# Kernel optimization log

Hardware: AMD Instinct MI355X
Metric: run time of the kernel (lower is better)

The kernel has to match this reference:

```python
import jax, jax.numpy as jnp
import numpy as np

N_NODES = 50000
N_EDGES = 1600000
NODE_DIM = 64
HIDDEN_DIM = 128
EDGE_DIM = 32


def _linear_params(key, fan_in, fan_out, bias=True):
    k1, k2 = jax.random.split(key)
    bound = 1.0 / np.sqrt(fan_in)
    W = jax.random.uniform(k1, (fan_in, fan_out), minval=-bound, maxval=bound, dtype=jnp.float32)
    if bias:
        b = jax.random.uniform(k2, (fan_out,), minval=-bound, maxval=bound, dtype=jnp.float32)
        return W, b
    return W, None


def setup_inputs() -> dict:
    key = jax.random.key(0)
    ks = jax.random.split(key, 12)
    h = jax.random.normal(ks[0], (N_NODES, NODE_DIM), dtype=jnp.float32)
    x = jax.random.normal(ks[1], (N_NODES, 3), dtype=jnp.float32) * 10.0
    edge_index = jax.random.randint(ks[2], (2, N_EDGES), 0, N_NODES, dtype=jnp.int32).astype(jnp.int64)
    edge_dist = jax.random.uniform(ks[3], (N_EDGES,), dtype=jnp.float32) * 10.0

    msg_in = 2 * NODE_DIM + EDGE_DIM
    node_w1, node_b1 = _linear_params(ks[4], msg_in, HIDDEN_DIM)
    node_w2, node_b2 = _linear_params(ks[5], HIDDEN_DIM, NODE_DIM)
    coord_w1, coord_b1 = _linear_params(ks[6], msg_in, HIDDEN_DIM)
    coord_w2, _ = _linear_params(ks[7], HIDDEN_DIM, 1, bias=False)
    edge_w1, edge_b1 = _linear_params(ks[8], 1, EDGE_DIM)
    edge_w2, edge_b2 = _linear_params(ks[9], EDGE_DIM, EDGE_DIM)

    return dict(h=h, x=x, edge_index=edge_index, edge_dist=edge_dist,
                node_w1=node_w1, node_b1=node_b1, node_w2=node_w2, node_b2=node_b2,
                coord_w1=coord_w1, coord_b1=coord_b1, coord_w2=coord_w2,
                edge_w1=edge_w1, edge_b1=edge_b1, edge_w2=edge_w2, edge_b2=edge_b2)


def reference(h, x, edge_index, edge_dist,
              node_w1, node_b1, node_w2, node_b2,
              coord_w1, coord_b1, coord_w2,
              edge_w1, edge_b1, edge_w2, edge_b2):
    src = edge_index[0]
    dst = edge_index[1]

    # edge_mlp: Linear(1, edge_dim) -> SiLU -> Linear(edge_dim, edge_dim)
    edge_attr = jax.nn.silu(edge_dist[:, None] @ edge_w1 + edge_b1) @ edge_w2 + edge_b2

    # per-edge message input: [E, 2*node_dim + edge_dim]
    m_input = jnp.concatenate([h[src], h[dst], edge_attr], axis=-1)

    # node_mlp: Linear -> SiLU -> Linear
    m = jax.nn.silu(m_input @ node_w1 + node_b1) @ node_w2 + node_b2
    h_agg = jnp.zeros_like(h).at[dst].add(m)

    # coord_mlp: Linear -> SiLU -> Linear(hidden, 1, bias=False)
    coord_weight = jax.nn.silu(m_input @ coord_w1 + coord_b1) @ coord_w2  # [E, 1]

    dir_vec = x[src] - x[dst]                               # [E, 3]
    dir_len = jnp.maximum(jnp.linalg.norm(dir_vec, axis=-1, keepdims=True), 1e-8)
    coord_update = coord_weight * (dir_vec / dir_len)
    x_agg = jnp.zeros_like(x).at[dst].add(coord_update)

    return (h + h_agg, x + x_agg)
```

## Files before the change

### kernel.cpp

```cpp
#include <hip/hip_runtime.h>
#include <stdint.h>

#define NN 50000
#define NE 1600000
#define BE 128

typedef __attribute__((ext_vector_type(8))) short short8;
typedef __attribute__((ext_vector_type(4))) float f32x4;

__device__ __forceinline__ unsigned short f2bf(float f) {
    unsigned int u = __float_as_uint(f);
    u += 0x7fff + ((u >> 16) & 1);
    return (unsigned short)(u >> 16);
}

__device__ __forceinline__ float silu_f(float v) {
    return v / (1.0f + __expf(-v));
}

__global__ void prep_kernel(const float* __restrict__ nw1,
                            const float* __restrict__ cw1,
                            const float* __restrict__ nw2,
                            unsigned short* __restrict__ ws) {
    int i = blockIdx.x * 256 + threadIdx.x;
    if (i < 20480) {
        int n = i / 160, k = i % 160;
        ws[i] = f2bf(nw1[k * 128 + n]);
    } else if (i < 40960) {
        int j = i - 20480; int n = j / 160, k = j % 160;
        ws[i] = f2bf(cw1[k * 128 + n]);
    } else if (i < 49152) {
        int j = i - 40960; int o = j / 128, k = j % 128;
        ws[i] = f2bf(nw2[k * 64 + o]);
    }
}

__global__ void init_out(const float4* __restrict__ h4,
                         const float4* __restrict__ x4,
                         float4* __restrict__ out4) {
    int i = blockIdx.x * 256 + threadIdx.x;
    if (i < 800000)       out4[i] = h4[i];
    else if (i < 837500)  out4[i] = x4[i - 800000];
}

#define MIS 168

__global__ __launch_bounds__(256, 2)
void egnn_edge_kernel(const float* __restrict__ h,
                      const float* __restrict__ x,
                      const int* __restrict__ eidx,
                      const float* __restrict__ edist,
                      const float* __restrict__ node_b1,
                      const float* __restrict__ node_b2,
                      const float* __restrict__ coord_b1,
                      const float* __restrict__ coord_w2,
                      const float* __restrict__ ew1,
                      const float* __restrict__ eb1,
                      const float* __restrict__ ew2,
                      const float* __restrict__ eb2,
                      const unsigned short* __restrict__ ws,
                      float* __restrict__ out_h,
                      float* __restrict__ out_x) {
    __shared__ unsigned short mi[BE * MIS];
    __shared__ unsigned short wbuf[64 * MIS];

    const int tid  = threadIdx.x;
    const int w    = tid >> 6;
    const int lane = tid & 63;
    const int ln   = lane & 15;
    const int quad = lane >> 4;
    const int e0   = blockIdx.x * BE;

    {
        const float4* h4 = (const float4*)h;
        const int g = tid >> 4, l16 = tid & 15;
        #pragma unroll
        for (int it = 0; it < 16; ++it) {
            int row = it * 16 + g;
            int e = row & 127;
            int node = (row < 128) ? eidx[e0 + e] : eidx[NE + e0 + e];
            int cbase = (row < 128) ? 0 : 64;
            float4 v = h4[node * 16 + l16];
            unsigned short b[4] = {f2bf(v.x), f2bf(v.y), f2bf(v.z), f2bf(v.w)};
            *(uint2*)&mi[e * MIS + cbase + l16 * 4] = *(uint2*)b;
        }
    }
    {
        int e = tid >> 1, half = tid & 1;
        float d = edist[e0 + e];
        float s[16];
        #pragma unroll
        for (int jj = 0; jj < 16; ++jj) s[jj] = eb2[half * 16 + jj];
        #pragma unroll
        for (int k = 0; k < 32; ++k) {
            float tk = silu_f(d * ew1[k] + eb1[k]);
            const float* r2 = ew2 + k * 32 + half * 16;
            #pragma unroll
            for (int jj = 0; jj < 16; ++jj) s[jj] += tk * r2[jj];
        }
        #pragma unroll
        for (int jj = 0; jj < 16; ++jj)
            mi[e * MIS + 128 + half * 16 + jj] = f2bf(s[jj]);
    }

    f32x4 accN[2][8], accC[2][8];
    const f32x4 zero = {0.f, 0.f, 0.f, 0.f};
    #pragma unroll
    for (int a = 0; a < 2; ++a)
        #pragma unroll
        for (int b = 0; b < 8; ++b) { accN[a][b] = zero; accC[a][b] = zero; }

    const int arow0 = (w * 32 + ln) * MIS;
    const int arow1 = (w * 32 + 16 + ln) * MIS;
    const int koff  = quad * 8;

    #pragma unroll
    for (int pass = 0; pass < 4; ++pass) {
        const int mat = pass >> 1, half = pass & 1;
        const unsigned short* wsrc = ws + mat * 20480 + half * 64 * 160;
        __syncthreads();
        #pragma unroll
        for (int c = 0; c < 5; ++c) {
            int idx = c * 256 + tid;
            int row = idx / 20, col8 = idx % 20;
            *(uint4*)&wbuf[row * MIS + col8 * 8] =
                *(const uint4*)(wsrc + row * 160 + col8 * 8);
        }
        __syncthreads();
        #pragma unroll
        for (int kc = 0; kc < 5; ++kc) {
            short8 a0 = *(const short8*)&mi[arow0 + kc * 32 + koff];
            short8 a1 = *(const short8*)&mi[arow1 + kc * 32 + koff];
            #pragma unroll
            for (int nt = 0; nt < 4; ++nt) {
                short8 b = *(const short8*)&wbuf[(nt * 16 + ln) * MIS + kc * 32 + koff];
                const int nn = half * 4 + nt;
                if (mat == 0) {
                    accN[0][nn] = __builtin_amdgcn_mfma_f32_16x16x32_bf16(a0, b, accN[0][nn], 0, 0, 0);
                    accN[1][nn] = __builtin_amdgcn_mfma_f32_16x16x32_bf16(a1, b, accN[1][nn], 0, 0, 0);
                } else {
                    accC[0][nn] = __builtin_amdgcn_mfma_f32_16x16x32_bf16(a0, b, accC[0][nn], 0, 0, 0);
                    accC[1][nn] = __builtin_amdgcn_mfma_f32_16x16x32_bf16(a1, b, accC[1][nn], 0, 0, 0);
                }
            }
        }
    }

    __syncthreads();
    #pragma unroll
    for (int mt = 0; mt < 2; ++mt) {
        const int rowb = (w * 32 + mt * 16 + quad * 4) * MIS;
        #pragma unroll
        for (int nt = 0; nt < 8; ++nt) {
            int col = nt * 16 + ln;
            float b1v = node_b1[col];
            #pragma unroll
            for (int r = 0; r < 4; ++r)
                mi[rowb + r * MIS + col] = f2bf(silu_f(accN[mt][nt][r] + b1v));
        }
    }
    __syncthreads();

    f32x4 acc2[2][4];
    #pragma unroll
    for (int a = 0; a < 2; ++a)
        #pragma unroll
        for (int b = 0; b < 4; ++b) acc2[a][b] = zero;
    const unsigned short* nw2T = ws + 40960;
    #pragma unroll
    for (int kc = 0; kc < 4; ++kc) {
        short8 a0 = *(const short8*)&mi[arow0 + kc * 32 + koff];
        short8 a1 = *(const short8*)&mi[arow1 + kc * 32 + koff];
        #pragma unroll
        for (int nt = 0; nt < 4; ++nt) {
            short8 b = *(const short8*)(nw2T + (nt * 16 + ln) * 128 + kc * 32 + koff);
            acc2[0][nt] = __builtin_amdgcn_mfma_f32_16x16x32_bf16(a0, b, acc2[0][nt], 0, 0, 0);
            acc2[1][nt] = __builtin_amdgcn_mfma_f32_16x16x32_bf16(a1, b, acc2[1][nt], 0, 0, 0);
        }
    }
    #pragma unroll
    for (int mt = 0; mt < 2; ++mt) {
        #pragma unroll
        for (int r = 0; r < 4; ++r) {
            int lrow = w * 32 + mt * 16 + quad * 4 + r;
            int dn = eidx[NE + e0 + lrow];
            float* outrow = out_h + (size_t)dn * 64;
            #pragma unroll
            for (int nt = 0; nt < 4; ++nt) {
                int col = nt * 16 + ln;
                atomicAdd(outrow + col, acc2[mt][nt][r] + node_b2[col]);
            }
        }
    }

    float cw[2][4];
    #pragma unroll
    for (int mt = 0; mt < 2; ++mt)
        #pragma unroll
        for (int r = 0; r < 4; ++r) cw[mt][r] = 0.f;
    #pragma unroll
    for (int nt = 0; nt < 8; ++nt) {
        int col = nt * 16 + ln;
        float b1v = coord_b1[col];
        float w2v = coord_w2[col];
        #pragma unroll
        for (int mt = 0; mt < 2; ++mt)
            #pragma unroll
            for (int r = 0; r < 4; ++r)
                cw[mt][r] += silu_f(accC[mt][nt][r] + b1v) * w2v;
    }
    #pragma unroll
    for (int off = 1; off < 16; off <<= 1) {
        #pragma unroll
        for (int mt = 0; mt < 2; ++mt)
            #pragma unroll
            for (int r = 0; r < 4; ++r)
                cw[mt][r] += __shfl_xor(cw[mt][r], off, 64);
    }
    if (ln < 8) {
        const int smt = ln >> 2, sr = ln & 3;
        float cwsel = 0.f;
        #pragma unroll
        for (int mt = 0; mt < 2; ++mt)
            #pragma unroll
            for (int r = 0; r < 4; ++r)
                cwsel = (mt == smt && r == sr) ? cw[mt][r] : cwsel;
        int lrow = w * 32 + smt * 16 + quad * 4 + sr;
        int s = eidx[e0 + lrow], dn = eidx[NE + e0 + lrow];
        float dx = x[s * 3]     - x[dn * 3];
        float dy = x[s * 3 + 1] - x[dn * 3 + 1];
        float dz = x[s * 3 + 2] - x[dn * 3 + 2];
        float len = fmaxf(sqrtf(dx * dx + dy * dy + dz * dz), 1e-8f);
        float k = cwsel / len;
        atomicAdd(out_x + dn * 3,     k * dx);
        atomicAdd(out_x + dn * 3 + 1, k * dy);
        atomicAdd(out_x + dn * 3 + 2, k * dz);
    }
}

extern "C" void kernel_launch(void* const* d_in, const int* in_sizes, int n_in,
                              void* d_out, int out_size, void* d_ws, size_t ws_size,
                              hipStream_t stream) {
    const float* h    = (const float*)d_in[0];
    const float* x    = (const float*)d_in[1];
    const int*   eidx = (const int*)d_in[2];
    const float* edist= (const float*)d_in[3];
    const float* nw1  = (const float*)d_in[4];
    const float* nb1  = (const float*)d_in[5];
    const float* nw2  = (const float*)d_in[6];
    const float* nb2  = (const float*)d_in[7];
    const float* cw1  = (const float*)d_in[8];
    const float* cb1  = (const float*)d_in[9];
    const float* cw2  = (const float*)d_in[10];
    const float* ew1  = (const float*)d_in[11];
    const float* eb1  = (const float*)d_in[12];
    const float* ew2  = (const float*)d_in[13];
    const float* eb2  = (const float*)d_in[14];
    float* out = (float*)d_out;
    unsigned short* ws = (unsigned short*)d_ws;

    prep_kernel<<<192, 256, 0, stream>>>(nw1, cw1, nw2, ws);
    init_out<<<3272, 256, 0, stream>>>((const float4*)h, (const float4*)x, (float4*)out);
    egnn_edge_kernel<<<NE / BE, 256, 0, stream>>>(h, x, eidx, edist,
                                                  nb1, nb2, cb1, cw2,
                                                  ew1, eb1, ew2, eb2,
                                                  ws, out, out + 3200000);
}
```

Measured before the change: 823.9 us.

## Pre-convert node features to bf16, read weights from global, drop LDS weight staging

Adds a prep kernel that converts h to a bf16 copy in the workspace, so each edge block gathers half as many bytes with 16-byte loads and does no conversion. The weight tiles are no longer staged through shared memory: the MFMA B operands are read straight from global/L2, and the node and coord matrices are processed in the same loop over halves. Coord accumulators are reduced per half to save registers, which allows raising launch bounds to 3 blocks per CU. This removes several barriers and LDS capacity use, at the cost of repeated global weight loads and one extra full pass over h.

New measurement: 1.118 ms. 35.7% more time.

```diff
diff --git a/kernel.cpp b/kernel.cpp
--- a/kernel.cpp
+++ b/kernel.cpp
@@ -18,10 +18,10 @@
     return v / (1.0f + __expf(-v));
 }
 
-__global__ void prep_kernel(const float* __restrict__ nw1,
-                            const float* __restrict__ cw1,
-                            const float* __restrict__ nw2,
-                            unsigned short* __restrict__ ws) {
+__global__ void prep_w(const float* __restrict__ nw1,
+                       const float* __restrict__ cw1,
+                       const float* __restrict__ nw2,
+                       unsigned short* __restrict__ ws) {
     int i = blockIdx.x * 256 + threadIdx.x;
     if (i < 20480) {
         int n = i / 160, k = i % 160;
@@ -35,6 +35,16 @@
     }
 }
 
+__global__ void prep_h(const float4* __restrict__ h4,
+                       unsigned short* __restrict__ hbf) {
+    int i = blockIdx.x * 256 + threadIdx.x;
+    if (i < 800000) {
+        float4 v = h4[i];
+        unsigned short b[4] = {f2bf(v.x), f2bf(v.y), f2bf(v.z), f2bf(v.w)};
+        *(uint2*)&hbf[i * 4] = *(uint2*)b;
+    }
+}
+
 __global__ void init_out(const float4* __restrict__ h4,
                          const float4* __restrict__ x4,
                          float4* __restrict__ out4) {
@@ -45,9 +55,8 @@
 
 #define MIS 168
 
-__global__ __launch_bounds__(256, 2)
-void egnn_edge_kernel(const float* __restrict__ h,
-                      const float* __restrict__ x,
+__global__ __launch_bounds__(256, 3)
+void egnn_edge_kernel(const float* __restrict__ x,
                       const int* __restrict__ eidx,
                       const float* __restrict__ edist,
                       const float* __restrict__ node_b1,
@@ -62,7 +71,6 @@
                       float* __restrict__ out_h,
                       float* __restrict__ out_x) {
     __shared__ unsigned short mi[BE * MIS];
-    __shared__ unsigned short wbuf[64 * MIS];
 
     const int tid  = threadIdx.x;
     const int w    = tid >> 6;
@@ -70,20 +78,17 @@
     const int ln   = lane & 15;
     const int quad = lane >> 4;
     const int e0   = blockIdx.x * BE;
-
-    {
-        const float4* h4 = (const float4*)h;
-        const int g = tid >> 4, l16 = tid & 15;
-        #pragma unroll
-        for (int it = 0; it < 16; ++it) {
-            int row = it * 16 + g;
-            int e = row & 127;
-            int node = (row < 128) ? eidx[e0 + e] : eidx[NE + e0 + e];
-            int cbase = (row < 128) ? 0 : 64;
-            float4 v = h4[node * 16 + l16];
-            unsigned short b[4] = {f2bf(v.x), f2bf(v.y), f2bf(v.z), f2bf(v.w)};
-            *(uint2*)&mi[e * MIS + cbase + l16 * 4] = *(uint2*)b;
-        }
+    const unsigned short* hbf = ws + 65536;
+
+    #pragma unroll
+    for (int it = 0; it < 8; ++it) {
+        int idx = it * 256 + tid;
+        int row = idx >> 3, chunk = idx & 7;
+        int e = row & 127;
+        int node = (row < 128) ? eidx[e0 + e] : eidx[NE + e0 + e];
+        int cbase = (row < 128) ? 0 : 64;
+        *(uint4*)&mi[e * MIS + cbase + chunk * 8] =
+            *(const uint4*)&hbf[node * 64 + chunk * 8];
     }
     {
         int e = tid >> 1, half = tid & 1;
@@ -102,51 +107,61 @@
         for (int jj = 0; jj < 16; ++jj)
             mi[e * MIS + 128 + half * 16 + jj] = f2bf(s[jj]);
     }
-
-    f32x4 accN[2][8], accC[2][8];
+    __syncthreads();
+
+    f32x4 accN[2][8];
     const f32x4 zero = {0.f, 0.f, 0.f, 0.f};
     #pragma unroll
     for (int a = 0; a < 2; ++a)
         #pragma unroll
-        for (int b = 0; b < 8; ++b) { accN[a][b] = zero; accC[a][b] = zero; }
+        for (int b = 0; b < 8; ++b) accN[a][b] = zero;
+    float cw[2][4];
+    #pragma unroll
+    for (int mt = 0; mt < 2; ++mt)
+        #pragma unroll
+        for (int r = 0; r < 4; ++r) cw[mt][r] = 0.f;
 
     const int arow0 = (w * 32 + ln) * MIS;
     const int arow1 = (w * 32 + 16 + ln) * MIS;
     const int koff  = quad * 8;
 
     #pragma unroll
-    for (int pass = 0; pass < 4; ++pass) {
-        const int mat = pass >> 1, half = pass & 1;
-        const unsigned short* wsrc = ws + mat * 20480 + half * 64 * 160;
-        __syncthreads();
-        #pragma unroll
-        for (int c = 0; c < 5; ++c) {
-            int idx = c * 256 + tid;
-            int row = idx / 20, col8 = idx % 20;
-            *(uint4*)&wbuf[row * MIS + col8 * 8] =
-                *(const uint4*)(wsrc + row * 160 + col8 * 8);
-        }
-        __syncthreads();
+    for (int half = 0; half < 2; ++half) {
+        f32x4 accC[2][4];
+        #pragma unroll
+        for (int a = 0; a < 2; ++a)
+            #pragma unroll
+            for (int b = 0; b < 4; ++b) accC[a][b] = zero;
         #pragma unroll
         for (int kc = 0; kc < 5; ++kc) {
             short8 a0 = *(const short8*)&mi[arow0 + kc * 32 + koff];
             short8 a1 = *(const short8*)&mi[arow1 + kc * 32 + koff];
             #pragma unroll
             for (int nt = 0; nt < 4; ++nt) {
-                short8 b = *(const short8*)&wbuf[(nt * 16 + ln) * MIS + kc * 32 + koff];
+                const unsigned short* bp =
+                    ws + (half * 64 + nt * 16 + ln) * 160 + kc * 32 + koff;
+                short8 bN = *(const short8*)bp;
+                short8 bC = *(const short8*)(bp + 20480);
                 const int nn = half * 4 + nt;
-                if (mat == 0) {
-                    accN[0][nn] = __builtin_amdgcn_mfma_f32_16x16x32_bf16(a0, b, accN[0][nn], 0, 0, 0);
-                    accN[1][nn] = __builtin_amdgcn_mfma_f32_16x16x32_bf16(a1, b, accN[1][nn], 0, 0, 0);
-                } else {
-                    accC[0][nn] = __builtin_amdgcn_mfma_f32_16x16x32_bf16(a0, b, accC[0][nn], 0, 0, 0);
-                    accC[1][nn] = __builtin_amdgcn_mfma_f32_16x16x32_bf16(a1, b, accC[1][nn], 0, 0, 0);
-                }
+                accN[0][nn] = __builtin_amdgcn_mfma_f32_16x16x32_bf16(a0, bN, accN[0][nn], 0, 0, 0);
+                accN[1][nn] = __builtin_amdgcn_mfma_f32_16x16x32_bf16(a1, bN, accN[1][nn], 0, 0, 0);
+                accC[0][nt] = __builtin_amdgcn_mfma_f32_16x16x32_bf16(a0, bC, accC[0][nt], 0, 0, 0);
+                accC[1][nt] = __builtin_amdgcn_mfma_f32_16x16x32_bf16(a1, bC, accC[1][nt], 0, 0, 0);
             }
         }
-    }
-
-    __syncthreads();
+        #pragma unroll
+        for (int nt = 0; nt < 4; ++nt) {
+            int col = half * 64 + nt * 16 + ln;
+            float b1v = coord_b1[col];
+            float w2v = coord_w2[col];
+            #pragma unroll
+            for (int mt = 0; mt < 2; ++mt)
+                #pragma unroll
+                for (int r = 0; r < 4; ++r)
+                    cw[mt][r] += silu_f(accC[mt][nt][r] + b1v) * w2v;
+        }
+    }
+
     #pragma unroll
     for (int mt = 0; mt < 2; ++mt) {
         const int rowb = (w * 32 + mt * 16 + quad * 4) * MIS;
@@ -159,7 +174,6 @@
                 mi[rowb + r * MIS + col] = f2bf(silu_f(accN[mt][nt][r] + b1v));
         }
     }
-    __syncthreads();
 
     f32x4 acc2[2][4];
     #pragma unroll
@@ -193,22 +207,6 @@
         }
     }
 
-    float cw[2][4];
-    #pragma unroll
-    for (int mt = 0; mt < 2; ++mt)
-        #pragma unroll
-        for (int r = 0; r < 4; ++r) cw[mt][r] = 0.f;
-    #pragma unroll
-    for (int nt = 0; nt < 8; ++nt) {
-        int col = nt * 16 + ln;
-        float b1v = coord_b1[col];
-        float w2v = coord_w2[col];
-        #pragma unroll
-        for (int mt = 0; mt < 2; ++mt)
-            #pragma unroll
-            for (int r = 0; r < 4; ++r)
-                cw[mt][r] += silu_f(accC[mt][nt][r] + b1v) * w2v;
-    }
     #pragma unroll
     for (int off = 1; off < 16; off <<= 1) {
         #pragma unroll
@@ -259,9 +257,10 @@
     float* out = (float*)d_out;
     unsigned short* ws = (unsigned short*)d_ws;
 
-    prep_kernel<<<192, 256, 0, stream>>>(nw1, cw1, nw2, ws);
+    prep_w<<<192, 256, 0, stream>>>(nw1, cw1, nw2, ws);
+    prep_h<<<3125, 256, 0, stream>>>((const float4*)h, ws + 65536);
     init_out<<<3272, 256, 0, stream>>>((const float4*)h, (const float4*)x, (float4*)out);
-    egnn_edge_kernel<<<NE / BE, 256, 0, stream>>>(h, x, eidx, edist,
+    egnn_edge_kernel<<<NE / BE, 256, 0, stream>>>(x, eidx, edist,
                                                   nb1, nb2, cb1, cw2,
                                                   ew1, eb1, ew2, eb2,
                                                   ws, out, out + 3200000);
```
